# Kernel optimization log

Hardware: AMD Instinct MI355X
Metric: run time of the kernel (lower is better)

The kernel has to match this reference:

```python
import jax, jax.numpy as jnp
import numpy as np

N_ITEMS = 100000
H = 256
L = 3
B = 512


def setup_inputs() -> dict:
    key = jax.random.key(0)
    ks = jax.random.split(key, 9)
    s = 1.0 / np.sqrt(H)  # PyTorch GRU/Linear default uniform bound
    return {
        "input": jax.random.randint(ks[0], (B,), 0, N_ITEMS),
        "hidden": jnp.zeros((L, B, H), jnp.float32),
        "W_ih0": jax.random.uniform(ks[1], (3 * H, N_ITEMS), jnp.float32, -s, s),
        "W_ih_hi": jax.random.uniform(ks[2], (L - 1, 3 * H, H), jnp.float32, -s, s),
        "W_hh": jax.random.uniform(ks[3], (L, 3 * H, H), jnp.float32, -s, s),
        "b_ih": jax.random.uniform(ks[4], (L, 3 * H), jnp.float32, -s, s),
        "b_hh": jax.random.uniform(ks[5], (L, 3 * H), jnp.float32, -s, s),
        "W_out": jax.random.uniform(ks[6], (N_ITEMS, H), jnp.float32, -s, s),
        "b_out": jax.random.uniform(ks[7], (N_ITEMS,), jnp.float32, -s, s),
    }


def _gru_cell(x_proj, h, W_hh_l, b_hh_l):
    # PyTorch GRU cell; x_proj already holds x @ W_ih.T + b_ih
    h_proj = h @ W_hh_l.T + b_hh_l
    xr, xz, xn = jnp.split(x_proj, 3, axis=-1)
    hr, hz, hn = jnp.split(h_proj, 3, axis=-1)
    r = jax.nn.sigmoid(xr + hr)
    z = jax.nn.sigmoid(xz + hz)
    n = jnp.tanh(xn + r * hn)
    return (1.0 - z) * n + z * h


def reference(input, hidden, W_ih0, W_ih_hi, W_hh, b_ih, b_hh, W_out, b_out):
    # one_hot(input) @ W_ih0.T == row-gather of W_ih0.T  (same math, no dense one-hot)
    x_proj = W_ih0.T[input] + b_ih[0]  # (B, 3H)
    x = _gru_cell(x_proj, hidden[0], W_hh[0], b_hh[0])
    new_h = [x]
    for l in range(1, L):  # fixed small layer loop
        x_proj = x @ W_ih_hi[l - 1].T + b_ih[l]
        x = _gru_cell(x_proj, hidden[l], W_hh[l], b_hh[l])
        new_h.append(x)
    h_new = jnp.stack(new_h)  # (L, B, H)
    activation = jnp.tanh(x @ W_out.T + b_out)  # (B, N_ITEMS)
    return activation, h_new
```

## Files before the change

kernel.cpp:

```cpp
#include <hip/hip_runtime.h>
#include <math.h>
#include <stdint.h>

#define NI 100000
#define NB 512
#define NH 256
#define H3 768

typedef _Float16 f16x8 __attribute__((ext_vector_type(8)));
typedef float    f32x4 __attribute__((ext_vector_type(4)));

__device__ __forceinline__ float tanh_fast(float x) {
    x = fminf(fmaxf(x, -9.0f), 9.0f);
    const float e = __expf(2.0f * x);
    return (e - 1.0f) * __builtin_amdgcn_rcpf(e + 1.0f);
}

__global__ void k_gates0(const int* __restrict__ idx,
                         const float* __restrict__ Wih0,
                         const float* __restrict__ bih0,
                         const float* __restrict__ hp,
                         const float* __restrict__ hprev,
                         float* __restrict__ hnew)
{
    const int b = blockIdx.x;
    const int j = threadIdx.x;
    const int ib = idx[b];
    const float xr = Wih0[(size_t)(j          ) * NI + ib] + bih0[j];
    const float xz = Wih0[(size_t)(j + NH     ) * NI + ib] + bih0[j + NH];
    const float xn = Wih0[(size_t)(j + 2 * NH ) * NI + ib] + bih0[j + 2 * NH];
    const float hr = hp[b * H3 + j];
    const float hz = hp[b * H3 + NH + j];
    const float hn = hp[b * H3 + 2 * NH + j];
    const float h  = hprev[b * NH + j];
    const float r = 1.0f / (1.0f + expf(-(xr + hr)));
    const float z = 1.0f / (1.0f + expf(-(xz + hz)));
    const float n = tanhf(xn + r * hn);
    hnew[b * NH + j] = (1.0f - z) * n + z * h;
}

__global__ void k_gates(const float* __restrict__ xp,
                        const float* __restrict__ hp,
                        const float* __restrict__ hprev,
                        float* __restrict__ hnew)
{
    const int b = blockIdx.x;
    const int j = threadIdx.x;
    const float xr = xp[b * H3 + j];
    const float xz = xp[b * H3 + NH + j];
    const float xn = xp[b * H3 + 2 * NH + j];
    const float hr = hp[b * H3 + j];
    const float hz = hp[b * H3 + NH + j];
    const float hn = hp[b * H3 + 2 * NH + j];
    const float h  = hprev[b * NH + j];
    const float r = 1.0f / (1.0f + expf(-(xr + hr)));
    const float z = 1.0f / (1.0f + expf(-(xz + hz)));
    const float n = tanhf(xn + r * hn);
    hnew[b * NH + j] = (1.0f - z) * n + z * h;
}

__global__ void k_gates_last(const float* __restrict__ xp,
                             const float* __restrict__ hp,
                             const float* __restrict__ hprev,
                             float* __restrict__ hnew,
                             _Float16* __restrict__ Xh)
{
    const int b = blockIdx.x;
    const int j = threadIdx.x;
    const float xr = xp[b * H3 + j];
    const float xz = xp[b * H3 + NH + j];
    const float xn = xp[b * H3 + 2 * NH + j];
    const float hr = hp[b * H3 + j];
    const float hz = hp[b * H3 + NH + j];
    const float hn = hp[b * H3 + 2 * NH + j];
    const float h  = hprev[b * NH + j];
    const float r = 1.0f / (1.0f + expf(-(xr + hr)));
    const float z = 1.0f / (1.0f + expf(-(xz + hz)));
    const float n = tanhf(xn + r * hn);
    const float v = (1.0f - z) * n + z * h;
    hnew[b * NH + j] = v;
    Xh[b * NH + j] = (_Float16)v;
}

__global__ __launch_bounds__(256)
void k_gemm_small(const float* __restrict__ A0,
                  const float* __restrict__ B0,
                  const float* __restrict__ bias0,
                  float* __restrict__ C0,
                  int M, int N, int K,
                  int sA, int sB, int sBias, int sC)
{
    constexpr int BM = 64, BN = 64, BK = 32;
    __shared__ float As[BK][BM];
    __shared__ float Bs[BK][BN];

    const float* A    = A0 + (size_t)blockIdx.z * sA;
    const float* Bm   = B0 + (size_t)blockIdx.z * sB;
    const float* bias = bias0 + (size_t)blockIdx.z * sBias;
    float*       C    = C0 + (size_t)blockIdx.z * sC;

    const int tid = threadIdx.x;
    const int tx  = tid & 15;
    const int ty  = tid >> 4;
    const int m0  = blockIdx.x * BM;
    const int n0  = blockIdx.y * BN;

    float acc[4][4];
#pragma unroll
    for (int i = 0; i < 4; i++)
#pragma unroll
        for (int j = 0; j < 4; j++) acc[i][j] = 0.0f;

    for (int k0 = 0; k0 < K; k0 += BK) {
#pragma unroll
        for (int f = 0; f < 2; f++) {
            const int fid = tid + f * 256;
            const int row = fid >> 3;
            const int t4  = fid & 7;
            const int mp  = row ^ ((t4 & 3) << 3);
            {
                const float4 v = *(const float4*)(A + (size_t)(m0 + row) * K + k0 + t4 * 4);
                As[t4 * 4 + 0][mp] = v.x; As[t4 * 4 + 1][mp] = v.y;
                As[t4 * 4 + 2][mp] = v.z; As[t4 * 4 + 3][mp] = v.w;
            }
            {
                const float4 v = *(const float4*)(Bm + (size_t)(n0 + row) * K + k0 + t4 * 4);
                Bs[t4 * 4 + 0][mp] = v.x; Bs[t4 * 4 + 1][mp] = v.y;
                Bs[t4 * 4 + 2][mp] = v.z; Bs[t4 * 4 + 3][mp] = v.w;
            }
        }
        __syncthreads();
#pragma unroll
        for (int kk = 0; kk < BK; kk++) {
            const int s = ((kk >> 2) & 3) << 3;
            const float4 a0 = *(const float4*)&As[kk][(ty * 4) ^ s];
            const float4 b0 = *(const float4*)&Bs[kk][(tx * 4) ^ s];
            const float av[4] = {a0.x, a0.y, a0.z, a0.w};
            const float bv[4] = {b0.x, b0.y, b0.z, b0.w};
#pragma unroll
            for (int i = 0; i < 4; i++)
#pragma unroll
                for (int j = 0; j < 4; j++)
                    acc[i][j] = fmaf(av[i], bv[j], acc[i][j]);
        }
        __syncthreads();
    }

#pragma unroll
    for (int i = 0; i < 4; i++) {
        const size_t rowoff = (size_t)(m0 + ty * 4 + i) * N;
        const int gn = n0 + tx * 4;
        const float4 bb = *(const float4*)(bias + gn);
        float4 v;
        v.x = acc[i][0] + bb.x; v.y = acc[i][1] + bb.y;
        v.z = acc[i][2] + bb.z; v.w = acc[i][3] + bb.w;
        *(float4*)(C + rowoff + gn) = v;
    }
}

__global__ __launch_bounds__(512, 4)
void k_out_mfma(const _Float16* __restrict__ Xh,
                const float* __restrict__ W,
                const float* __restrict__ bout,
                float* __restrict__ C)
{
    __shared__ __align__(16) float S[16384];

    const int n0   = blockIdx.x * 64;
    const int tid  = threadIdx.x;
    const int w    = tid >> 6;
    const int lane = tid & 63;
    const int lr   = lane & 15;
    const int lg   = lane >> 4;

#pragma unroll
    for (int it = 0; it < 8; ++it) {
        const int fid = it * 512 + tid;
        const int row = fid >> 6;
        const int p   = fid & 63;
        int gr = n0 + row; if (gr >= NI) gr = NI - 1;
        const float* src = W + (size_t)gr * NH + (size_t)(p ^ (row & 7)) * 4;
        __builtin_amdgcn_global_load_lds(
            (const __attribute__((address_space(1))) void*)src,
            (__attribute__((address_space(3))) void*)(S + fid * 4),
            16, 0, 0);
    }

    f32x4 acc[4][4];
#pragma unroll
    for (int nf = 0; nf < 4; ++nf)
#pragma unroll
        for (int mf = 0; mf < 4; ++mf) acc[nf][mf] = (f32x4){0.f, 0.f, 0.f, 0.f};

    __syncthreads();

    const _Float16* xbase = Xh + (size_t)(w * 64 + lr) * NH + lg * 8;

#pragma unroll
    for (int t = 0; t < 8; ++t) {
        f16x8 xf[4];
#pragma unroll
        for (int mf = 0; mf < 4; ++mf)
            xf[mf] = *(const f16x8*)(xbase + mf * 16 * NH + t * 32);
#pragma unroll
        for (int nf = 0; nf < 4; ++nf) {
            const int rl = nf * 16 + lr;
            const int c0 = t * 8 + ((lg * 2)     ^ (rl & 7));
            const int c1 = t * 8 + ((lg * 2 + 1) ^ (rl & 7));
            const f32x4 u0 = *(const f32x4*)(S + rl * 256 + c0 * 4);
            const f32x4 u1 = *(const f32x4*)(S + rl * 256 + c1 * 4);
            f16x8 h;
            h[0] = (_Float16)u0[0]; h[1] = (_Float16)u0[1];
            h[2] = (_Float16)u0[2]; h[3] = (_Float16)u0[3];
            h[4] = (_Float16)u1[0]; h[5] = (_Float16)u1[1];
            h[6] = (_Float16)u1[2]; h[7] = (_Float16)u1[3];
#pragma unroll
            for (int mf = 0; mf < 4; ++mf)
                acc[nf][mf] = __builtin_amdgcn_mfma_f32_16x16x32_f16(
                    h, xf[mf], acc[nf][mf], 0, 0, 0);
        }
    }

#pragma unroll
    for (int pass = 0; pass < 2; ++pass) {
        __syncthreads();
        if ((w >> 2) == pass) {
            const int mloc = (w & 3) * 64;
#pragma unroll
            for (int nf = 0; nf < 4; ++nf) {
                const int gn = n0 + nf * 16 + lg * 4;
                const float4 bb = (gn < NI) ? *(const float4*)(bout + gn)
                                            : make_float4(0.f, 0.f, 0.f, 0.f);
#pragma unroll
                for (int mf = 0; mf < 4; ++mf) {
                    const int mr = mloc + mf * 16 + lr;
                    const int p  = (nf * 4 + lg) ^ (lr & 7);
                    float4 v;
                    v.x = tanh_fast(acc[nf][mf][0] + bb.x);
                    v.y = tanh_fast(acc[nf][mf][1] + bb.y);
                    v.z = tanh_fast(acc[nf][mf][2] + bb.z);
                    v.w = tanh_fast(acc[nf][mf][3] + bb.w);
                    *(float4*)(S + mr * 64 + p * 4) = v;
                }
            }
        }
        __syncthreads();
#pragma unroll
        for (int it = 0; it < 8; ++it) {
            const int fid = it * 512 + tid;
            const int row = fid >> 4;
            const int c   = fid & 15;
            const int gn  = n0 + c * 4;
            if (gn < NI) {
                const f32x4 v = *(const f32x4*)(S + row * 64 + ((c ^ (row & 7)) * 4));
                *(f32x4*)(C + (size_t)(pass * 256 + row) * NI + gn) = v;
            }
        }
    }
}

extern "C" void kernel_launch(void* const* d_in, const int* in_sizes, int n_in,
                              void* d_out, int out_size, void* d_ws, size_t ws_size,
                              hipStream_t stream)
{
    const int*   idx    = (const int*)  d_in[0];
    const float* hidden = (const float*)d_in[1];
    const float* Wih0   = (const float*)d_in[2];
    const float* WihHi  = (const float*)d_in[3];
    const float* Whh    = (const float*)d_in[4];
    const float* bih    = (const float*)d_in[5];
    const float* bhh    = (const float*)d_in[6];
    const float* Wout   = (const float*)d_in[7];
    const float* bout   = (const float*)d_in[8];

    float* act  = (float*)d_out;
    float* hnew = act + (size_t)NB * NI;
    float* hp = act;
    float* xp = act + 3 * NB * H3;
    _Float16* Xh = (_Float16*)d_ws;

    const dim3 bs(256);
    const dim3 gs_hp(NB / 64, H3 / 64, 3);
    const dim3 gs_xp(NB / 64, H3 / 64, 1);

    k_gemm_small<<<gs_hp, bs, 0, stream>>>(hidden, Whh, bhh, hp,
                                           NB, H3, NH, NB * NH, H3 * NH, H3, NB * H3);
    k_gates0<<<NB, bs, 0, stream>>>(idx, Wih0, bih, hp, hidden, hnew);
    k_gemm_small<<<gs_xp, bs, 0, stream>>>(hnew, WihHi, bih + H3, xp,
                                           NB, H3, NH, 0, 0, 0, 0);
    k_gates<<<NB, bs, 0, stream>>>(xp, hp + NB * H3, hidden + NB * NH, hnew + NB * NH);
    k_gemm_small<<<gs_xp, bs, 0, stream>>>(hnew + NB * NH, WihHi + H3 * NH, bih + 2 * H3, xp,
                                           NB, H3, NH, 0, 0, 0, 0);
    k_gates_last<<<NB, bs, 0, stream>>>(xp, hp + 2 * NB * H3, hidden + 2 * NB * NH,
                                        hnew + 2 * NB * NH, Xh);

    k_out_mfma<<<dim3((NI + 63) / 64), dim3(512), 0, stream>>>(Xh, Wout, bout, act);
}
```

Measured before the change: 180.9 us.

## Stage W_out tile as fp16 in LDS to halve shared memory and raise occupancy

The output projection kernel now loads W_out rows into registers, converts them to fp16 once, and writes a swizzled fp16 tile to LDS, replacing the async fp32 global-to-LDS copy. This halves the LDS footprint to 32KB and removes the repeated fp32-to-fp16 conversion inside the MFMA loop. The epilogue is reworked to write through a 32KB buffer in four passes of 128 rows, and launch bounds are raised to 8 blocks per CU. In exchange it loses the direct async LDS load, so global loads pass through registers, and it adds more barriers in the epilogue.

```diff
diff --git a/kernel.cpp b/kernel.cpp
--- a/kernel.cpp
+++ b/kernel.cpp
@@ -8,6 +8,7 @@
 #define H3 768
 
 typedef _Float16 f16x8 __attribute__((ext_vector_type(8)));
+typedef _Float16 f16x4 __attribute__((ext_vector_type(4)));
 typedef float    f32x4 __attribute__((ext_vector_type(4)));
 
 __device__ __forceinline__ float tanh_fast(float x) {
@@ -158,13 +159,14 @@
     }
 }
 
-__global__ __launch_bounds__(512, 4)
+__global__ __launch_bounds__(512, 8)
 void k_out_mfma(const _Float16* __restrict__ Xh,
                 const float* __restrict__ W,
                 const float* __restrict__ bout,
                 float* __restrict__ C)
 {
-    __shared__ __align__(16) float S[16384];
+    __shared__ __align__(16) _Float16 S16[64 * 256];
+    float* Cs = (float*)S16;
 
     const int n0   = blockIdx.x * 64;
     const int tid  = threadIdx.x;
@@ -173,17 +175,26 @@
     const int lr   = lane & 15;
     const int lg   = lane >> 4;
 
+    float4 stg[8];
 #pragma unroll
     for (int it = 0; it < 8; ++it) {
         const int fid = it * 512 + tid;
         const int row = fid >> 6;
-        const int p   = fid & 63;
+        const int c32 = fid & 63;
         int gr = n0 + row; if (gr >= NI) gr = NI - 1;
-        const float* src = W + (size_t)gr * NH + (size_t)(p ^ (row & 7)) * 4;
-        __builtin_amdgcn_global_load_lds(
-            (const __attribute__((address_space(1))) void*)src,
-            (__attribute__((address_space(3))) void*)(S + fid * 4),
-            16, 0, 0);
+        stg[it] = *(const float4*)(W + (size_t)gr * NH + c32 * 4);
+    }
+#pragma unroll
+    for (int it = 0; it < 8; ++it) {
+        const int fid = it * 512 + tid;
+        const int row = fid >> 6;
+        const int c32 = fid & 63;
+        const int s   = c32 >> 1;
+        const int ps  = (s & 24) | ((s ^ row) & 7);
+        f16x4 h;
+        h[0] = (_Float16)stg[it].x; h[1] = (_Float16)stg[it].y;
+        h[2] = (_Float16)stg[it].z; h[3] = (_Float16)stg[it].w;
+        *(f16x4*)((char*)S16 + row * 512 + ps * 16 + (c32 & 1) * 8) = h;
     }
 
     f32x4 acc[4][4];
@@ -205,27 +216,22 @@
 #pragma unroll
         for (int nf = 0; nf < 4; ++nf) {
             const int rl = nf * 16 + lr;
-            const int c0 = t * 8 + ((lg * 2)     ^ (rl & 7));
-            const int c1 = t * 8 + ((lg * 2 + 1) ^ (rl & 7));
-            const f32x4 u0 = *(const f32x4*)(S + rl * 256 + c0 * 4);
-            const f32x4 u1 = *(const f32x4*)(S + rl * 256 + c1 * 4);
-            f16x8 h;
-            h[0] = (_Float16)u0[0]; h[1] = (_Float16)u0[1];
-            h[2] = (_Float16)u0[2]; h[3] = (_Float16)u0[3];
-            h[4] = (_Float16)u1[0]; h[5] = (_Float16)u1[1];
-            h[6] = (_Float16)u1[2]; h[7] = (_Float16)u1[3];
+            const int s  = t * 4 + lg;
+            const int ps = (s & 24) | ((s ^ rl) & 7);
+            const f16x8 wf = *(const f16x8*)((const char*)S16 + rl * 512 + ps * 16);
 #pragma unroll
             for (int mf = 0; mf < 4; ++mf)
                 acc[nf][mf] = __builtin_amdgcn_mfma_f32_16x16x32_f16(
-                    h, xf[mf], acc[nf][mf], 0, 0, 0);
-        }
-    }
-
-#pragma unroll
-    for (int pass = 0; pass < 2; ++pass) {
-        __syncthreads();
-        if ((w >> 2) == pass) {
-            const int mloc = (w & 3) * 64;
+                    wf, xf[mf], acc[nf][mf], 0, 0, 0);
+        }
+    }
+
+    __syncthreads();
+    const int myp = w >> 1;
+#pragma unroll
+    for (int p = 0; p < 4; ++p) {
+        if (p) __syncthreads();
+        if (myp == p) {
 #pragma unroll
             for (int nf = 0; nf < 4; ++nf) {
                 const int gn = n0 + nf * 16 + lg * 4;
@@ -233,27 +239,29 @@
                                             : make_float4(0.f, 0.f, 0.f, 0.f);
 #pragma unroll
                 for (int mf = 0; mf < 4; ++mf) {
-                    const int mr = mloc + mf * 16 + lr;
-                    const int p  = (nf * 4 + lg) ^ (lr & 7);
+                    const int lrow = (w & 1) * 64 + mf * 16 + lr;
+                    const int q    = nf * 4 + lg;
+                    const int pq   = (q & 8) | ((q ^ lrow) & 7);
                     float4 v;
                     v.x = tanh_fast(acc[nf][mf][0] + bb.x);
                     v.y = tanh_fast(acc[nf][mf][1] + bb.y);
                     v.z = tanh_fast(acc[nf][mf][2] + bb.z);
                     v.w = tanh_fast(acc[nf][mf][3] + bb.w);
-                    *(float4*)(S + mr * 64 + p * 4) = v;
+                    *(float4*)(Cs + lrow * 64 + pq * 4) = v;
                 }
             }
         }
         __syncthreads();
 #pragma unroll
-        for (int it = 0; it < 8; ++it) {
+        for (int it = 0; it < 4; ++it) {
             const int fid = it * 512 + tid;
             const int row = fid >> 4;
-            const int c   = fid & 15;
-            const int gn  = n0 + c * 4;
+            const int q   = fid & 15;
+            const int pq  = (q & 8) | ((q ^ row) & 7);
+            const int gn  = n0 + q * 4;
             if (gn < NI) {
-                const f32x4 v = *(const f32x4*)(S + row * 64 + ((c ^ (row & 7)) * 4));
-                *(f32x4*)(C + (size_t)(pass * 256 + row) * NI + gn) = v;
+                const f32x4 v = *(const f32x4*)(Cs + row * 64 + pq * 4);
+                *(f32x4*)(C + (size_t)(p * 128 + row) * NI + gn) = v;
             }
         }
     }
```

Result: slower. 526.9 us (+191.3%).

## Make output GEMM persistent with double-buffered LDS prefetch of W_out tiles

Applied to the files above, without the earlier changes.

The output projection kernel now runs a fixed grid of 256 persistent blocks. Each block loops over 64-row tiles of W_out and prefetches the next tile into a second LDS buffer while computing the current one. The goal is to hide global load latency and cut block launch overhead. The cost is double the LDS per block (128KB) and a lower launch-bounds occupancy, which leaves roughly one block per CU and less overlap between blocks.

```diff
diff --git a/kernel.cpp b/kernel.cpp
--- a/kernel.cpp
+++ b/kernel.cpp
@@ -6,6 +6,8 @@
 #define NB 512
 #define NH 256
 #define H3 768
+#define NT 1563
+#define GRID_OUT 256
 
 typedef _Float16 f16x8 __attribute__((ext_vector_type(8)));
 typedef float    f32x4 __attribute__((ext_vector_type(4)));
@@ -158,104 +160,118 @@
     }
 }
 
-__global__ __launch_bounds__(512, 4)
+__global__ __launch_bounds__(512, 2)
 void k_out_mfma(const _Float16* __restrict__ Xh,
                 const float* __restrict__ W,
                 const float* __restrict__ bout,
                 float* __restrict__ C)
 {
-    __shared__ __align__(16) float S[16384];
-
-    const int n0   = blockIdx.x * 64;
+    __shared__ __align__(16) float Wbuf[2][64 * 256];
+
     const int tid  = threadIdx.x;
     const int w    = tid >> 6;
     const int lane = tid & 63;
     const int lr   = lane & 15;
     const int lg   = lane >> 4;
 
-#pragma unroll
-    for (int it = 0; it < 8; ++it) {
-        const int fid = it * 512 + tid;
-        const int row = fid >> 6;
-        const int p   = fid & 63;
-        int gr = n0 + row; if (gr >= NI) gr = NI - 1;
-        const float* src = W + (size_t)gr * NH + (size_t)(p ^ (row & 7)) * 4;
-        __builtin_amdgcn_global_load_lds(
-            (const __attribute__((address_space(1))) void*)src,
-            (__attribute__((address_space(3))) void*)(S + fid * 4),
-            16, 0, 0);
-    }
-
-    f32x4 acc[4][4];
-#pragma unroll
-    for (int nf = 0; nf < 4; ++nf)
-#pragma unroll
-        for (int mf = 0; mf < 4; ++mf) acc[nf][mf] = (f32x4){0.f, 0.f, 0.f, 0.f};
-
-    __syncthreads();
-
     const _Float16* xbase = Xh + (size_t)(w * 64 + lr) * NH + lg * 8;
 
-#pragma unroll
-    for (int t = 0; t < 8; ++t) {
-        f16x8 xf[4];
-#pragma unroll
-        for (int mf = 0; mf < 4; ++mf)
-            xf[mf] = *(const f16x8*)(xbase + mf * 16 * NH + t * 32);
-#pragma unroll
-        for (int nf = 0; nf < 4; ++nf) {
-            const int rl = nf * 16 + lr;
-            const int c0 = t * 8 + ((lg * 2)     ^ (rl & 7));
-            const int c1 = t * 8 + ((lg * 2 + 1) ^ (rl & 7));
-            const f32x4 u0 = *(const f32x4*)(S + rl * 256 + c0 * 4);
-            const f32x4 u1 = *(const f32x4*)(S + rl * 256 + c1 * 4);
-            f16x8 h;
-            h[0] = (_Float16)u0[0]; h[1] = (_Float16)u0[1];
-            h[2] = (_Float16)u0[2]; h[3] = (_Float16)u0[3];
-            h[4] = (_Float16)u1[0]; h[5] = (_Float16)u1[1];
-            h[6] = (_Float16)u1[2]; h[7] = (_Float16)u1[3];
-#pragma unroll
-            for (int mf = 0; mf < 4; ++mf)
-                acc[nf][mf] = __builtin_amdgcn_mfma_f32_16x16x32_f16(
-                    h, xf[mf], acc[nf][mf], 0, 0, 0);
-        }
-    }
-
-#pragma unroll
-    for (int pass = 0; pass < 2; ++pass) {
-        __syncthreads();
-        if ((w >> 2) == pass) {
-            const int mloc = (w & 3) * 64;
-#pragma unroll
-            for (int nf = 0; nf < 4; ++nf) {
-                const int gn = n0 + nf * 16 + lg * 4;
-                const float4 bb = (gn < NI) ? *(const float4*)(bout + gn)
-                                            : make_float4(0.f, 0.f, 0.f, 0.f);
-#pragma unroll
-                for (int mf = 0; mf < 4; ++mf) {
-                    const int mr = mloc + mf * 16 + lr;
-                    const int p  = (nf * 4 + lg) ^ (lr & 7);
-                    float4 v;
-                    v.x = tanh_fast(acc[nf][mf][0] + bb.x);
-                    v.y = tanh_fast(acc[nf][mf][1] + bb.y);
-                    v.z = tanh_fast(acc[nf][mf][2] + bb.z);
-                    v.w = tanh_fast(acc[nf][mf][3] + bb.w);
-                    *(float4*)(S + mr * 64 + p * 4) = v;
-                }
-            }
-        }
-        __syncthreads();
+    auto stage = [&](float* buf, int ny) {
 #pragma unroll
         for (int it = 0; it < 8; ++it) {
             const int fid = it * 512 + tid;
-            const int row = fid >> 4;
-            const int c   = fid & 15;
-            const int gn  = n0 + c * 4;
-            if (gn < NI) {
-                const f32x4 v = *(const f32x4*)(S + row * 64 + ((c ^ (row & 7)) * 4));
-                *(f32x4*)(C + (size_t)(pass * 256 + row) * NI + gn) = v;
-            }
-        }
+            const int row = fid >> 6;
+            const int p   = fid & 63;
+            int gr = ny * 64 + row; if (gr >= NI) gr = NI - 1;
+            const float* src = W + (size_t)gr * NH + (size_t)(p ^ (row & 7)) * 4;
+            __builtin_amdgcn_global_load_lds(
+                (const __attribute__((address_space(1))) void*)src,
+                (__attribute__((address_space(3))) void*)(buf + fid * 4),
+                16, 0, 0);
+        }
+    };
+
+    stage(Wbuf[0], blockIdx.x);
+    __syncthreads();
+    int cur = 0;
+
+    for (int t = blockIdx.x; t < NT; t += GRID_OUT) {
+        const int n0 = t * 64;
+        if (t + GRID_OUT < NT) stage(Wbuf[cur ^ 1], t + GRID_OUT);
+
+        f32x4 acc[4][4];
+#pragma unroll
+        for (int nf = 0; nf < 4; ++nf)
+#pragma unroll
+            for (int mf = 0; mf < 4; ++mf) acc[nf][mf] = (f32x4){0.f, 0.f, 0.f, 0.f};
+
+        const float* S = Wbuf[cur];
+#pragma unroll
+        for (int tt = 0; tt < 8; ++tt) {
+            f16x8 xf[4];
+#pragma unroll
+            for (int mf = 0; mf < 4; ++mf)
+                xf[mf] = *(const f16x8*)(xbase + mf * 16 * NH + tt * 32);
+#pragma unroll
+            for (int nf = 0; nf < 4; ++nf) {
+                const int rl = nf * 16 + lr;
+                const int c0 = tt * 8 + ((lg * 2)     ^ (rl & 7));
+                const int c1 = tt * 8 + ((lg * 2 + 1) ^ (rl & 7));
+                const f32x4 u0 = *(const f32x4*)(S + rl * 256 + c0 * 4);
+                const f32x4 u1 = *(const f32x4*)(S + rl * 256 + c1 * 4);
+                f16x8 h;
+                h[0] = (_Float16)u0[0]; h[1] = (_Float16)u0[1];
+                h[2] = (_Float16)u0[2]; h[3] = (_Float16)u0[3];
+                h[4] = (_Float16)u1[0]; h[5] = (_Float16)u1[1];
+                h[6] = (_Float16)u1[2]; h[7] = (_Float16)u1[3];
+#pragma unroll
+                for (int mf = 0; mf < 4; ++mf)
+                    acc[nf][mf] = __builtin_amdgcn_mfma_f32_16x16x32_f16(
+                        h, xf[mf], acc[nf][mf], 0, 0, 0);
+            }
+        }
+
+        __syncthreads();
+
+        float* Cs = Wbuf[cur];
+#pragma unroll
+        for (int p2 = 0; p2 < 2; ++p2) {
+            if ((w >> 2) == p2) {
+                const int mloc = (w & 3) * 64;
+#pragma unroll
+                for (int nf = 0; nf < 4; ++nf) {
+                    const int gn = n0 + nf * 16 + lg * 4;
+                    const float4 bb = (gn < NI) ? *(const float4*)(bout + gn)
+                                                : make_float4(0.f, 0.f, 0.f, 0.f);
+#pragma unroll
+                    for (int mf = 0; mf < 4; ++mf) {
+                        const int mr = mloc + mf * 16 + lr;
+                        const int ps = (nf * 4 + lg) ^ (lr & 7);
+                        float4 v;
+                        v.x = tanh_fast(acc[nf][mf][0] + bb.x);
+                        v.y = tanh_fast(acc[nf][mf][1] + bb.y);
+                        v.z = tanh_fast(acc[nf][mf][2] + bb.z);
+                        v.w = tanh_fast(acc[nf][mf][3] + bb.w);
+                        *(float4*)(Cs + mr * 64 + ps * 4) = v;
+                    }
+                }
+            }
+            __syncthreads();
+#pragma unroll
+            for (int it = 0; it < 8; ++it) {
+                const int fid = it * 512 + tid;
+                const int row = fid >> 4;
+                const int c   = fid & 15;
+                const int pq  = c ^ (row & 7);
+                const int gn  = n0 + c * 4;
+                if (gn < NI) {
+                    const f32x4 v = *(const f32x4*)(Cs + row * 64 + pq * 4);
+                    *(f32x4*)(C + (size_t)(p2 * 256 + row) * NI + gn) = v;
+                }
+            }
+            __syncthreads();
+        }
+        cur ^= 1;
     }
 }
 
@@ -294,5 +310,5 @@
     k_gates_last<<<NB, bs, 0, stream>>>(xp, hp + 2 * NB * H3, hidden + 2 * NB * NH,
                                         hnew + 2 * NB * NH, Xh);
 
-    k_out_mfma<<<dim3((NI + 63) / 64), dim3(512), 0, stream>>>(Xh, Wout, bout, act);
-}
+    k_out_mfma<<<dim3(GRID_OUT), dim3(512), 0, stream>>>(Xh, Wout, bout, act);
+}
```

Result: slower. 221.6 us (+22.5%).
